# Kernel optimization log

Hardware: AMD Instinct MI355X
Metric: run time of the kernel (lower is better)

Reference implementation:

```python
import jax, jax.numpy as jnp
import numpy as np

T_BINS = 1000  # max_time_bins
N_HEADS = 8
BIN = 64


def _ln(x, g, b):
    m = x.mean(-1, keepdims=True)
    v = ((x - m) ** 2).mean(-1, keepdims=True)
    return (x - m) / jnp.sqrt(v + 1e-5) * g + b


def _time_attn(h, td, mask, wq, bq, wk, bk, wv, bv, wo, bo, temb):
    # h: [B,S,D], td: [B,S] float, mask: [B,S] bool
    B, S, D = h.shape
    dk = D // N_HEADS
    q = (h @ wq + bq).reshape(B, S, N_HEADS, dk)
    k = (h @ wk + bk).reshape(B, S, N_HEADS, dk)
    v = (h @ wv + bv).reshape(B, S, N_HEADS, dk)
    scores = jnp.einsum('bqhd,bkhd->bhqk', q, k) / jnp.sqrt(jnp.float32(dk))
    tb = jnp.clip(td.astype(jnp.int32), 0, T_BINS - 1)
    bias = temb[tb].transpose(0, 2, 1)[:, :, None, :]  # [B,H,1,S], key-position bias
    scores = jnp.where(mask[:, None, None, :], scores + bias, -1e9)
    attn = jax.nn.softmax(scores, axis=-1)
    ctx = jnp.einsum('bhqk,bkhd->bqhd', attn, v).reshape(B, S, D)
    return ctx @ wo + bo


def _forward(x, time_deltas,
             emb_event, emb_rel, emb_abs,
             iq_w, iq_b, ik_w, ik_b, iv_w, iv_b, io_w, io_b, i_temb, i_g, i_bt,
             eq_w, eq_b, ek_w, ek_b, ev_w, ev_b, eo_w, eo_b, e_temb, e_g, e_bt,
             w1, b1, w2, b2):
    B, S = x.shape
    NB = S // BIN  # S chosen as a multiple of bin_size -> no padding
    mask = x != 0  # padding_idx = 0
    ee = emb_event.at[0].set(0.0)  # padding_idx row is zero
    rel_bins = jnp.clip(time_deltas.astype(jnp.int32), 0, T_BINS - 1)
    abs_t = jnp.cumsum(jnp.clip(time_deltas, 0.0, None), axis=1)
    abs_bins = jnp.clip(abs_t.astype(jnp.int32), 0, T_BINS - 1)
    h = ee[x] + emb_rel[rel_bins] + emb_abs[abs_bins]  # [B,S,D]
    D = h.shape[-1]
    # intra-bin attention over [B*NB, BIN]
    hi = h.reshape(B * NB, BIN, D)
    ti = time_deltas.reshape(B * NB, BIN)
    mi = mask.reshape(B * NB, BIN)
    hi = _ln(_time_attn(hi, ti, mi, iq_w, iq_b, ik_w, ik_b, iv_w, iv_b, io_w, io_b, i_temb), i_g, i_bt)
    hi = hi.reshape(B, NB, BIN, D)
    # mean pool per bin over valid tokens
    mb = mask.reshape(B, NB, BIN)
    w = mb[..., None].astype(h.dtype)
    denom = jnp.maximum(w.sum(2), 1.0)
    bin_repr = (hi * w).sum(2) / denom  # [B,NB,D]
    bin_mask = mb.any(2)
    abs_masked = jnp.where(mb, abs_t.reshape(B, NB, BIN), 0.0)
    bin_abs = abs_masked.max(2)
    bin_rel = jnp.concatenate(
        [jnp.zeros((B, 1), h.dtype), jnp.maximum(bin_abs[:, 1:] - bin_abs[:, :-1], 0.0)], axis=1)
    h_inter = _ln(_time_attn(bin_repr, bin_rel, bin_mask,
                             eq_w, eq_b, ek_w, ek_b, ev_w, ev_b, eo_w, eo_b, e_temb), e_g, e_bt)
    last_idx = jnp.clip(bin_mask.sum(1) - 1, 0, None)
    last = h_inter[jnp.arange(B), last_idx]  # [B,D]
    return jax.nn.sigmoid(jax.nn.relu(last @ w1 + b1) @ w2 + b2)  # [B,1]


def setup_inputs() -> dict:
    key = jax.random.key(0)
    ks = jax.random.split(key, 24)
    B, S, D, V = 8, 4096, 512, 20000
    sc = 1.0 / np.sqrt(D)
    f32 = jnp.float32
    inp = {
        'x': jax.random.randint(ks[0], (B, S), 0, V),
        'time_deltas': jax.random.uniform(ks[1], (B, S), f32) * 10.0,
        'emb_event': jax.random.normal(ks[2], (V, D), f32) * 0.02,
        'emb_rel': jax.random.normal(ks[3], (T_BINS, D), f32) * 0.02,
        'emb_abs': jax.random.normal(ks[4], (T_BINS, D), f32) * 0.02,
    }
    names = ['iq', 'ik', 'iv', 'io', 'eq', 'ek', 'ev', 'eo']
    for i, n in enumerate(names):
        inp[n + '_w'] = jax.random.normal(ks[5 + i], (D, D), f32) * sc
        inp[n + '_b'] = jnp.zeros((D,), f32)
    inp['i_temb'] = jax.random.normal(ks[13], (T_BINS, N_HEADS), f32) * 0.02
    inp['e_temb'] = jax.random.normal(ks[14], (T_BINS, N_HEADS), f32) * 0.02
    inp['i_g'] = jnp.ones((D,), f32); inp['i_bt'] = jnp.zeros((D,), f32)
    inp['e_g'] = jnp.ones((D,), f32); inp['e_bt'] = jnp.zeros((D,), f32)
    inp['w1'] = jax.random.normal(ks[15], (D, D // 2), f32) * sc
    inp['b1'] = jnp.zeros((D // 2,), f32)
    inp['w2'] = jax.random.normal(ks[16], (D // 2, 1), f32) * np.sqrt(2.0 / D)
    inp['b2'] = jnp.zeros((1,), f32)
    return inp


def reference(x, time_deltas, emb_event, emb_rel, emb_abs,
              iq_w, iq_b, ik_w, ik_b, iv_w, iv_b, io_w, io_b, i_temb, i_g, i_bt,
              eq_w, eq_b, ek_w, ek_b, ev_w, ev_b, eo_w, eo_b, e_temb, e_g, e_bt,
              w1, b1, w2, b2):
    return _forward(x, time_deltas, emb_event, emb_rel, emb_abs,
                    iq_w, iq_b, ik_w, ik_b, iv_w, iv_b, io_w, io_b, i_temb, i_g, i_bt,
                    eq_w, eq_b, ek_w, ek_b, ev_w, ev_b, eo_w, eo_b, e_temb, e_g, e_bt,
                    w1, b1, w2, b2)
```

## Files before the change

kernel.cpp:

```cpp
#include <hip/hip_runtime.h>


typedef __attribute__((ext_vector_type(8))) short bf16x8;
typedef __attribute__((ext_vector_type(4))) float f32x4;
typedef __attribute__((ext_vector_type(4))) int i32x4;

#define DEVI __device__ __forceinline__

DEVI unsigned short f2bf(float f) {
  union { float f; unsigned u; } v; v.f = f;
  unsigned r = v.u + 0x7FFFu + ((v.u >> 16) & 1u);
  return (unsigned short)(r >> 16);
}
DEVI float bf2f(unsigned short u) {
  union { unsigned u; float f; } v; v.u = ((unsigned)u) << 16; return v.f;
}

#define GLOAD_LDS16(gp, lp) \
  __builtin_amdgcn_global_load_lds((const __attribute__((address_space(1))) void*)(gp), \
                                   (__attribute__((address_space(3))) void*)(lp), 16, 0, 0)

struct TPackArgs { const float* s[8]; unsigned short* d[8];
                   const float* bs[6]; float* bd[2]; };

__global__ __launch_bounds__(256) void k_tpack8(TPackArgs args) {
  __shared__ float tile[64][65];
  if (blockIdx.x == 512) {
    int t = threadIdx.x;
    for (int i = t; i < 1536; i += 256) {
      int sel = i >> 9, r = i & 511;
      args.bd[0][i] = args.bs[sel][r];
      args.bd[1][i] = args.bs[3 + sel][r];
    }
    return;
  }
  int mat = blockIdx.x >> 6;
  int tl = blockIdx.x & 63;
  const float* W = args.s[mat];
  unsigned short* Wt = args.d[mat];
  int n0 = (tl & 7) << 6, k0 = (tl >> 3) << 6;
  int t = threadIdx.x, j = t & 63, i0 = t >> 6;
#pragma unroll
  for (int rr = 0; rr < 16; ++rr) {
    int i = rr * 4 + i0;
    tile[i][j] = W[(size_t)(k0 + i) * 512 + n0 + j];
  }
  __syncthreads();
#pragma unroll
  for (int rr = 0; rr < 16; ++rr) {
    int i = rr * 4 + i0;
    Wt[(size_t)(n0 + i) * 512 + k0 + j] = f2bf(tile[j][i]);
  }
}

__global__ __launch_bounds__(64) void k_time(const float* __restrict__ td, const int* __restrict__ x,
    float* __restrict__ abs_t, float* __restrict__ bin_rel, int* __restrict__ bin_mask,
    int* __restrict__ last_idx) {
  __shared__ float tds[4096];
  __shared__ int xs[4096];
  int b = blockIdx.x, lane = threadIdx.x;
  const f32x4* tp = (const f32x4*)(td + (size_t)b * 4096);
  const i32x4* xp = (const i32x4*)(x + (size_t)b * 4096);
  for (int j = lane; j < 1024; j += 64) {
    f32x4 v = tp[j];
#pragma unroll
    for (int c = 0; c < 4; ++c) v[c] = fmaxf(v[c], 0.f);
    *(f32x4*)&tds[j * 4] = v;
    *(i32x4*)&xs[j * 4] = xp[j];
  }
  __syncthreads();
  float s = 0.f;
  for (int i = 0; i < 64; ++i) s += tds[lane * 64 + i];
  float pre = s;
#pragma unroll
  for (int off = 1; off < 64; off <<= 1) {
    float n = __shfl_up(pre, off, 64);
    if (lane >= off) pre += n;
  }
  float a = pre - s;
  float am = 0.f; int anyv = 0;
  for (int i = 0; i < 64; ++i) {
    a += tds[lane * 64 + i];
    tds[lane * 64 + i] = a;
    if (xs[lane * 64 + i] != 0) { am = fmaxf(am, a); anyv = 1; }
  }
  __syncthreads();
  float* out = abs_t + (size_t)b * 4096;
  for (int j = lane; j < 1024; j += 64)
    *(f32x4*)&out[j * 4] = *(const f32x4*)&tds[j * 4];
  float prev = __shfl_up(am, 1, 64);
  bin_rel[b * 64 + lane] = (lane == 0) ? 0.f : fmaxf(am - prev, 0.f);
  bin_mask[b * 64 + lane] = anyv;
  unsigned long long bal = __ballot(anyv != 0);
  if (lane == 0) last_idx[b] = max(__popcll(bal) - 1, 0);
}

__global__ __launch_bounds__(256) void k_embed(const int* __restrict__ x, const float* __restrict__ td,
    const float* __restrict__ abs_t, const float* __restrict__ ee, const float* __restrict__ er,
    const float* __restrict__ ea, unsigned short* __restrict__ h) {
  int t = threadIdx.x;
  int lane = t & 63;
  int c0 = lane * 8;
#pragma unroll
  for (int it = 0; it < 4; ++it) {
    int tok = blockIdx.x * 16 + it * 4 + (t >> 6);
    int xi = x[tok];
    int rb = (int)td[tok]; rb = min(max(rb, 0), 999);
    int ab = (int)abs_t[tok]; ab = min(max(ab, 0), 999);
    const f32x4* pr = (const f32x4*)(er + (size_t)rb * 512 + c0);
    const f32x4* pa = (const f32x4*)(ea + (size_t)ab * 512 + c0);
    f32x4 s0 = pr[0] + pa[0];
    f32x4 s1 = pr[1] + pa[1];
    if (xi != 0) {
      const f32x4* pe = (const f32x4*)(ee + (size_t)xi * 512 + c0);
      s0 += pe[0]; s1 += pe[1];
    }
    bf16x8 o;
#pragma unroll
    for (int i = 0; i < 4; ++i) { o[i] = (short)f2bf(s0[i]); o[4 + i] = (short)f2bf(s1[i]); }
    *(bf16x8*)(h + (size_t)tok * 512 + c0) = o;
  }
}

DEVI bf16x8 lds_frag32(const unsigned short* buf, int r, int g) {
  int sr = r >> 1;
  int slot = (((r & 1) << 2) | g) ^ (sr & 7);
  return *(const bf16x8*)&buf[sr * 64 + slot * 8];
}
DEVI bf16x8 lds_frag64(const unsigned short* buf, int row, int c) {
  return *(const bf16x8*)&buf[row * 64 + ((c ^ (row & 7)) << 3)];
}

__global__ __launch_bounds__(512, 2) void k_gemm256(const unsigned short* __restrict__ A,
    const unsigned short* __restrict__ Wt, const float* __restrict__ bias,
    unsigned short* __restrict__ Cout, int N, int tiles_n) {
  __shared__ unsigned short lds[4][2][256 * 32];
  int bid = blockIdx.x;
  { int q = (int)gridDim.x >> 3; bid = (bid & 7) * q + (bid >> 3); }
  int by = bid / tiles_n, bx = bid % tiles_n;
  int m0 = by << 8, n0 = bx << 8;
  int t = threadIdx.x;
  int lane = t & 63, w = t >> 6;
  int wm = w >> 2, wn = w & 3;
  int l15 = lane & 15, l4 = lane >> 4;

  auto stageA = [&](int kt) {
    int k0 = kt << 5;
    unsigned short* dst = &lds[kt & 3][0][0];
#pragma unroll
    for (int l = 0; l < 2; ++l) {
      int pos = l * 512 + t;
      int sr = pos >> 3, slot = pos & 7;
      int gp = slot ^ (sr & 7);
      int row = sr * 2 + (gp >> 2);
      GLOAD_LDS16(&A[(size_t)(m0 + row) * 512 + k0 + (gp & 3) * 8], dst + pos * 8);
    }
  };
  auto stageB = [&](int kt) {
    int k0 = kt << 5;
    unsigned short* dst = &lds[kt & 3][1][0];
#pragma unroll
    for (int l = 0; l < 2; ++l) {
      int pos = l * 512 + t;
      int sr = pos >> 3, slot = pos & 7;
      int gp = slot ^ (sr & 7);
      int row = sr * 2 + (gp >> 2);
      GLOAD_LDS16(&Wt[(size_t)(n0 + row) * 512 + k0 + (gp & 3) * 8], dst + pos * 8);
    }
  };

  f32x4 acc[8][4] = {};
  stageA(0); stageB(0);
  stageA(1); stageB(1);
  stageA(2); stageB(2);

  for (int kt = 0; kt < 16; ++kt) {
    if (kt < 14)       asm volatile("s_waitcnt vmcnt(8)" ::: "memory");
    else if (kt == 14) asm volatile("s_waitcnt vmcnt(4)" ::: "memory");
    else               asm volatile("s_waitcnt vmcnt(0)" ::: "memory");
    __builtin_amdgcn_s_barrier();
    const unsigned short* As = &lds[kt & 3][0][0];
    const unsigned short* Bs = &lds[kt & 3][1][0];

    bf16x8 af[4], bb[4];
#pragma unroll
    for (int i = 0; i < 4; ++i) af[i] = lds_frag32(As, wm * 128 + i * 16 + l15, l4);
#pragma unroll
    for (int j = 0; j < 4; ++j) bb[j] = lds_frag32(Bs, wn * 64 + j * 16 + l15, l4);
    if (kt < 13) stageA(kt + 3);
    __builtin_amdgcn_s_barrier();
    asm volatile("s_waitcnt lgkmcnt(0)" ::: "memory");
    __builtin_amdgcn_sched_barrier(0);
    __builtin_amdgcn_s_setprio(1);
#pragma unroll
    for (int i = 0; i < 4; ++i)
#pragma unroll
      for (int j = 0; j < 4; ++j)
        acc[i][j] = __builtin_amdgcn_mfma_f32_16x16x32_bf16(af[i], bb[j], acc[i][j], 0, 0, 0);
    __builtin_amdgcn_s_setprio(0);

    bf16x8 ah[4];
#pragma unroll
    for (int i = 0; i < 4; ++i) ah[i] = lds_frag32(As, wm * 128 + 64 + i * 16 + l15, l4);
    if (kt < 13) stageB(kt + 3);
    __builtin_amdgcn_s_barrier();
    asm volatile("s_waitcnt lgkmcnt(0)" ::: "memory");
    __builtin_amdgcn_sched_barrier(0);
    __builtin_amdgcn_s_setprio(1);
#pragma unroll
    for (int i = 0; i < 4; ++i)
#pragma unroll
      for (int j = 0; j < 4; ++j)
        acc[4 + i][j] = __builtin_amdgcn_mfma_f32_16x16x32_bf16(ah[i], bb[j], acc[4 + i][j], 0, 0, 0);
    __builtin_amdgcn_s_setprio(0);
  }

  __syncthreads();
  unsigned short* scr = ((unsigned short*)lds) + (size_t)w * 4352;
  float bov[4];
#pragma unroll
  for (int j = 0; j < 4; ++j) bov[j] = bias[n0 + wn * 64 + j * 16 + l15];
#pragma unroll
  for (int c = 0; c < 2; ++c) {
#pragma unroll
    for (int i = 0; i < 4; ++i)
#pragma unroll
      for (int j = 0; j < 4; ++j)
#pragma unroll
        for (int r = 0; r < 4; ++r)
          scr[(i * 16 + l4 * 4 + r) * 68 + j * 16 + l15] = f2bf(acc[c * 4 + i][j][r] + bov[j]);
#pragma unroll
    for (int p = 0; p < 8; ++p) {
      int rl = p * 8 + (lane >> 3);
      bf16x8 vv = *(const bf16x8*)&scr[rl * 68 + (lane & 7) * 8];
      *(bf16x8*)&Cout[(size_t)(m0 + wm * 128 + c * 64 + rl) * N + n0 + wn * 64 + (lane & 7) * 8] = vv;
    }
  }
}

__global__ __launch_bounds__(512, 2) void k_oproj(const unsigned short* __restrict__ ctx,
    const unsigned short* __restrict__ WoT, const float* __restrict__ bo,
    const int* __restrict__ x, const float* __restrict__ g, const float* __restrict__ bt,
    unsigned short* __restrict__ bin_repr) {
  __shared__ unsigned short As[128 * 64];
  __shared__ unsigned short Bs[512 * 64];
  int bid = blockIdx.x;
  { int q = (int)gridDim.x >> 3; bid = (bid & 7) * q + (bid >> 3); }
  int m0 = bid << 7;
  int t = threadIdx.x;
  int lane = t & 63, w = t >> 6;
  int l15 = lane & 15, l4 = lane >> 4;

  f32x4 acc[8][4] = {};
  for (int k0 = 0; k0 < 512; k0 += 64) {
    __syncthreads();
#pragma unroll
    for (int l = 0; l < 2; ++l) {
      int pos = l * 512 + t;
      int row = pos >> 3, gg = (pos & 7) ^ (row & 7);
      GLOAD_LDS16(&ctx[(size_t)(m0 + row) * 512 + k0 + gg * 8], &As[pos * 8]);
    }
#pragma unroll
    for (int l = 0; l < 8; ++l) {
      int pos = l * 512 + t;
      int row = pos >> 3, gg = (pos & 7) ^ (row & 7);
      GLOAD_LDS16(&WoT[(size_t)row * 512 + k0 + gg * 8], &Bs[pos * 8]);
    }
    __syncthreads();
#pragma unroll
    for (int ks = 0; ks < 2; ++ks) {
      bf16x8 af[8], bb[4];
#pragma unroll
      for (int i = 0; i < 8; ++i) af[i] = lds_frag64(As, i * 16 + l15, ks * 4 + l4);
#pragma unroll
      for (int j = 0; j < 4; ++j) bb[j] = lds_frag64(Bs, w * 64 + j * 16 + l15, ks * 4 + l4);
#pragma unroll
      for (int i = 0; i < 8; ++i)
#pragma unroll
        for (int j = 0; j < 4; ++j)
          acc[i][j] = __builtin_amdgcn_mfma_f32_16x16x32_bf16(af[i], bb[j], acc[i][j], 0, 0, 0);
    }
  }

  __syncthreads();
  float* red   = (float*)&As[0];
  float* meanL = red + 128 * 9;
  float* rstdL = meanL + 128;
  int*   valL  = (int*)(rstdL + 128);
  int*   cntL  = valL + 128;

  int cols[4]; float bov[4], gv[4], bv[4];
#pragma unroll
  for (int j = 0; j < 4; ++j) {
    cols[j] = w * 64 + j * 16 + l15;
    bov[j] = bo[cols[j]]; gv[j] = g[cols[j]]; bv[j] = bt[cols[j]];
  }
  if (t < 128) {
    int v = (x[m0 + t] != 0) ? 1 : 0;
    valL[t] = v;
    unsigned long long bal = __ballot(v != 0);
    if ((t & 63) == 0) cntL[t >> 6] = __popcll(bal);
  }
#pragma unroll
  for (int i = 0; i < 8; ++i)
#pragma unroll
    for (int r = 0; r < 4; ++r) {
      float s = (acc[i][0][r] + bov[0]) + (acc[i][1][r] + bov[1]) +
                (acc[i][2][r] + bov[2]) + (acc[i][3][r] + bov[3]);
#pragma unroll
      for (int off = 1; off < 16; off <<= 1) s += __shfl_xor(s, off, 64);
      if (l15 == 0) red[(i * 16 + l4 * 4 + r) * 9 + w] = s;
    }
  __syncthreads();
  if (t < 128) {
    float m = 0.f;
#pragma unroll
    for (int ww = 0; ww < 8; ++ww) m += red[t * 9 + ww];
    meanL[t] = m * (1.f / 512.f);
  }
  __syncthreads();
#pragma unroll
  for (int i = 0; i < 8; ++i)
#pragma unroll
    for (int r = 0; r < 4; ++r) {
      float m = meanL[i * 16 + l4 * 4 + r];
      float s = 0.f;
#pragma unroll
      for (int j = 0; j < 4; ++j) { float d = acc[i][j][r] + bov[j] - m; s += d * d; }
#pragma unroll
      for (int off = 1; off < 16; off <<= 1) s += __shfl_xor(s, off, 64);
      if (l15 == 0) red[(i * 16 + l4 * 4 + r) * 9 + w] = s;
    }
  __syncthreads();
  if (t < 128) {
    float vsum = 0.f;
#pragma unroll
    for (int ww = 0; ww < 8; ++ww) vsum += red[t * 9 + ww];
    rstdL[t] = rsqrtf(vsum * (1.f / 512.f) + 1e-5f);
  }
  __syncthreads();
  float p0[4] = {0.f, 0.f, 0.f, 0.f}, p1[4] = {0.f, 0.f, 0.f, 0.f};
#pragma unroll
  for (int i = 0; i < 8; ++i)
#pragma unroll
    for (int r = 0; r < 4; ++r) {
      int row = i * 16 + l4 * 4 + r;
      if (valL[row]) {
        float m = meanL[row], rs = rstdL[row];
#pragma unroll
        for (int j = 0; j < 4; ++j) {
          float y = (acc[i][j][r] + bov[j] - m) * rs * gv[j] + bv[j];
          if (i < 4) p0[j] += y; else p1[j] += y;
        }
      }
    }
#pragma unroll
  for (int j = 0; j < 4; ++j) {
    p0[j] += __shfl_xor(p0[j], 16, 64); p0[j] += __shfl_xor(p0[j], 32, 64);
    p1[j] += __shfl_xor(p1[j], 16, 64); p1[j] += __shfl_xor(p1[j], 32, 64);
  }
  float d0 = 1.f / fmaxf((float)cntL[0], 1.f);
  float d1 = 1.f / fmaxf((float)cntL[1], 1.f);
  if (l4 == 0) {
    int binr = (m0 >> 6);
#pragma unroll
    for (int j = 0; j < 4; ++j) {
      bin_repr[(size_t)binr * 512 + cols[j]]       = f2bf(p0[j] * d0);
      bin_repr[(size_t)(binr + 1) * 512 + cols[j]] = f2bf(p1[j] * d1);
    }
  }
}

__global__ __launch_bounds__(256) void k_gemm(const unsigned short* __restrict__ A,
    const unsigned short* __restrict__ Wt, const float* __restrict__ bias,
    unsigned short* __restrict__ Cout, int N, int tiles_n) {
  __shared__ unsigned short As[128 * 72];
  __shared__ unsigned short Bs[128 * 72];
  int bx = blockIdx.x % tiles_n;
  int by = blockIdx.x / tiles_n;
  int m0 = by << 7, n0 = bx << 7;
  int t = threadIdx.x;
  int lane = t & 63, w = t >> 6;
  int wm = w >> 1, wn = w & 1;
  f32x4 acc[4][4] = {};
  for (int k0 = 0; k0 < 512; k0 += 64) {
    __syncthreads();
#pragma unroll
    for (int i = 0; i < 4; ++i) {
      int idx = t + i * 256;
      int row = idx >> 3, seg = idx & 7;
      *(bf16x8*)&As[row * 72 + seg * 8] = *(const bf16x8*)&A[(size_t)(m0 + row) * 512 + k0 + seg * 8];
      *(bf16x8*)&Bs[row * 72 + seg * 8] = *(const bf16x8*)&Wt[(size_t)(n0 + row) * 512 + k0 + seg * 8];
    }
    __syncthreads();
#pragma unroll
    for (int ks = 0; ks < 2; ++ks) {
      bf16x8 af[4], bb[4];
#pragma unroll
      for (int i = 0; i < 4; ++i) {
        af[i] = *(const bf16x8*)&As[(wm * 64 + i * 16 + (lane & 15)) * 72 + ks * 32 + (lane >> 4) * 8];
        bb[i] = *(const bf16x8*)&Bs[(wn * 64 + i * 16 + (lane & 15)) * 72 + ks * 32 + (lane >> 4) * 8];
      }
#pragma unroll
      for (int i = 0; i < 4; ++i)
#pragma unroll
        for (int j = 0; j < 4; ++j)
          acc[i][j] = __builtin_amdgcn_mfma_f32_16x16x32_bf16(af[i], bb[j], acc[i][j], 0, 0, 0);
    }
  }
#pragma unroll
  for (int i = 0; i < 4; ++i) {
    int rowb = m0 + wm * 64 + i * 16 + ((lane >> 4) << 2);
#pragma unroll
    for (int j = 0; j < 4; ++j) {
      int col = n0 + wn * 64 + j * 16 + (lane & 15);
      float bv = bias[col];
#pragma unroll
      for (int r = 0; r < 4; ++r)
        Cout[(size_t)(rowb + r) * N + col] = f2bf(acc[i][j][r] + bv);
    }
  }
}

__global__ __launch_bounds__(256) void k_attn(const unsigned short* __restrict__ qkv,
    const float* __restrict__ td, const int* __restrict__ validv,
    const float* __restrict__ temb, unsigned short* __restrict__ ctx) {
  __shared__ float bias_s[4][64];
  __shared__ int valid_s[64];
  __shared__ unsigned short P_s[4][64][72];
  __shared__ unsigned short Vt_s[4][64][72];
  int blk = blockIdx.x >> 1, hg = blockIdx.x & 1;
  int t = threadIdx.x, hl = t >> 6, lane = t & 63;
  int h = hg * 4 + hl;
  size_t base = (size_t)blk * 64;
  if (t < 64) {
    valid_s[t] = (validv[base + t] != 0) ? 1 : 0;
    int tb = (int)td[base + t];
    tb = min(max(tb, 0), 999);
#pragma unroll
    for (int hh = 0; hh < 4; ++hh) bias_s[hh][t] = temb[tb * 8 + hg * 4 + hh];
  }
  {
    const unsigned short* vp = qkv + (base + lane) * 1536 + 1024 + h * 64;
#pragma unroll
    for (int f8 = 0; f8 < 8; ++f8) {
      bf16x8 v8 = *(const bf16x8*)(vp + f8 * 8);
#pragma unroll
      for (int j = 0; j < 8; ++j) Vt_s[hl][f8 * 8 + j][lane] = (unsigned short)v8[j];
    }
  }
  __syncthreads();
  bf16x8 qa[2][4], kb[2][4];
#pragma unroll
  for (int ks = 0; ks < 2; ++ks)
#pragma unroll
    for (int i = 0; i < 4; ++i) {
      int row = i * 16 + (lane & 15);
      int kk = ks * 32 + (lane >> 4) * 8;
      qa[ks][i] = *(const bf16x8*)&qkv[(base + row) * 1536 + h * 64 + kk];
      kb[ks][i] = *(const bf16x8*)&qkv[(base + row) * 1536 + 512 + h * 64 + kk];
    }
  f32x4 acc[4][4] = {};
#pragma unroll
  for (int ks = 0; ks < 2; ++ks)
#pragma unroll
    for (int i = 0; i < 4; ++i)
#pragma unroll
      for (int j = 0; j < 4; ++j)
        acc[i][j] = __builtin_amdgcn_mfma_f32_16x16x32_bf16(qa[ks][i], kb[ks][j], acc[i][j], 0, 0, 0);
  float invs[4][4];
#pragma unroll
  for (int i = 0; i < 4; ++i) {
#pragma unroll
    for (int r = 0; r < 4; ++r) {
      float sv[4];
#pragma unroll
      for (int j = 0; j < 4; ++j) {
        int key = j * 16 + (lane & 15);
        float s = acc[i][j][r] * 0.125f;
        sv[j] = valid_s[key] ? (s + bias_s[hl][key]) : -1e9f;
      }
      float m = fmaxf(fmaxf(sv[0], sv[1]), fmaxf(sv[2], sv[3]));
#pragma unroll
      for (int off = 1; off < 16; off <<= 1) m = fmaxf(m, __shfl_xor(m, off, 64));
      float p[4], sum = 0.f;
#pragma unroll
      for (int j = 0; j < 4; ++j) { p[j] = __expf(sv[j] - m); sum += p[j]; }
#pragma unroll
      for (int off = 1; off < 16; off <<= 1) sum += __shfl_xor(sum, off, 64);
      invs[i][r] = 1.f / sum;
      int row = i * 16 + ((lane >> 4) << 2) + r;
#pragma unroll
      for (int j = 0; j < 4; ++j) P_s[hl][row][j * 16 + (lane & 15)] = f2bf(p[j]);
    }
  }
  __syncthreads();
  f32x4 acc2[4][4] = {};
#pragma unroll
  for (int ks = 0; ks < 2; ++ks) {
    bf16x8 pa[4], vb[4];
    int kk = ks * 32 + (lane >> 4) * 8;
#pragma unroll
    for (int i = 0; i < 4; ++i) {
      pa[i] = *(const bf16x8*)&P_s[hl][i * 16 + (lane & 15)][kk];
      vb[i] = *(const bf16x8*)&Vt_s[hl][i * 16 + (lane & 15)][kk];
    }
#pragma unroll
    for (int i = 0; i < 4; ++i)
#pragma unroll
      for (int j = 0; j < 4; ++j)
        acc2[i][j] = __builtin_amdgcn_mfma_f32_16x16x32_bf16(pa[i], vb[j], acc2[i][j], 0, 0, 0);
  }
  unsigned short* scr = &Vt_s[hl][0][0];
#pragma unroll
  for (int i = 0; i < 4; ++i)
#pragma unroll
    for (int j = 0; j < 4; ++j)
#pragma unroll
      for (int r = 0; r < 4; ++r)
        scr[(i * 16 + ((lane >> 4) << 2) + r) * 72 + j * 16 + (lane & 15)] =
            f2bf(acc2[i][j][r] * invs[i][r]);
#pragma unroll
  for (int p = 0; p < 8; ++p) {
    int rl = p * 8 + (lane >> 3);
    bf16x8 vv = *(const bf16x8*)&scr[rl * 72 + (lane & 7) * 8];
    *(bf16x8*)&ctx[(base + rl) * 512 + h * 64 + (lane & 7) * 8] = vv;
  }
}

__global__ __launch_bounds__(256) void k_final(const unsigned short* __restrict__ proj2,
    const int* __restrict__ last_idx, const float* __restrict__ g, const float* __restrict__ bt,
    const float* __restrict__ w1, const float* __restrict__ b1,
    const float* __restrict__ w2, const float* __restrict__ b2, float* __restrict__ outp) {
  __shared__ float row_s[512];
  __shared__ float red_s[4];
  __shared__ float red2_s[4];
  int b = blockIdx.x, t = threadIdx.x;
  const unsigned short* rp = proj2 + (size_t)(b * 64 + last_idx[b]) * 512;
  float v0 = bf2f(rp[t]), v1 = bf2f(rp[t + 256]);
  float s = v0 + v1;
#pragma unroll
  for (int off = 1; off < 64; off <<= 1) s += __shfl_xor(s, off, 64);
  if ((t & 63) == 0) red_s[t >> 6] = s;
  __syncthreads();
  float mean = (red_s[0] + red_s[1] + red_s[2] + red_s[3]) * (1.f / 512.f);
  float d0 = v0 - mean, d1 = v1 - mean;
  float vs = d0 * d0 + d1 * d1;
#pragma unroll
  for (int off = 1; off < 64; off <<= 1) vs += __shfl_xor(vs, off, 64);
  if ((t & 63) == 0) red2_s[t >> 6] = vs;
  __syncthreads();
  float rstd = rsqrtf((red2_s[0] + red2_s[1] + red2_s[2] + red2_s[3]) * (1.f / 512.f) + 1e-5f);
  row_s[t]       = d0 * rstd * g[t]       + bt[t];
  row_s[t + 256] = d1 * rstd * g[t + 256] + bt[t + 256];
  __syncthreads();
  float acc = b1[t];
  for (int k = 0; k < 512; ++k) acc += row_s[k] * w1[(size_t)k * 256 + t];
  float hv = fmaxf(acc, 0.f) * w2[t];
#pragma unroll
  for (int off = 1; off < 64; off <<= 1) hv += __shfl_xor(hv, off, 64);
  if ((t & 63) == 0) red_s[t >> 6] = hv;
  __syncthreads();
  if (t == 0) {
    float o = red_s[0] + red_s[1] + red_s[2] + red_s[3] + b2[0];
    outp[b] = 1.f / (1.f + __expf(-o));
  }
}

extern "C" void kernel_launch(void* const* d_in, const int* in_sizes, int n_in,
                              void* d_out, int out_size, void* d_ws, size_t ws_size,
                              hipStream_t stream) {
  const int*   x    = (const int*)d_in[0];
  const float* td   = (const float*)d_in[1];
  const float* ee   = (const float*)d_in[2];
  const float* er   = (const float*)d_in[3];
  const float* ea   = (const float*)d_in[4];
  const float* iq_w = (const float*)d_in[5];  const float* iq_b = (const float*)d_in[6];
  const float* ik_w = (const float*)d_in[7];  const float* ik_b = (const float*)d_in[8];
  const float* iv_w = (const float*)d_in[9];  const float* iv_b = (const float*)d_in[10];
  const float* io_w = (const float*)d_in[11]; const float* io_b = (const float*)d_in[12];
  const float* eq_w = (const float*)d_in[13]; const float* eq_b = (const float*)d_in[14];
  const float* ek_w = (const float*)d_in[15]; const float* ek_b = (const float*)d_in[16];
  const float* ev_w = (const float*)d_in[17]; const float* ev_b = (const float*)d_in[18];
  const float* eo_w = (const float*)d_in[19]; const float* eo_b = (const float*)d_in[20];
  const float* i_temb = (const float*)d_in[21];
  const float* e_temb = (const float*)d_in[22];
  const float* i_g  = (const float*)d_in[23]; const float* i_bt = (const float*)d_in[24];
  const float* e_g  = (const float*)d_in[25]; const float* e_bt = (const float*)d_in[26];
  const float* w1   = (const float*)d_in[27]; const float* b1   = (const float*)d_in[28];
  const float* w2   = (const float*)d_in[29]; const float* b2   = (const float*)d_in[30];

  char* ws = (char*)d_ws;
  size_t off = 0;
  auto alloc = [&](size_t nb) { size_t r = off; off += (nb + 255) & ~(size_t)255; return r; };
  float* abs_t    = (float*)(ws + alloc((size_t)32768 * 4));
  float* bin_rel  = (float*)(ws + alloc(512 * 4));
  int*   bin_mask = (int*)(ws + alloc(512 * 4));
  int*   last_idx = (int*)(ws + alloc(64));
  unsigned short* wqkv_i = (unsigned short*)(ws + alloc((size_t)1536 * 512 * 2));
  unsigned short* wo_i   = (unsigned short*)(ws + alloc((size_t)512 * 512 * 2));
  unsigned short* wqkv_e = (unsigned short*)(ws + alloc((size_t)1536 * 512 * 2));
  unsigned short* wo_e   = (unsigned short*)(ws + alloc((size_t)512 * 512 * 2));
  float* bqkv_i = (float*)(ws + alloc(1536 * 4));
  float* bqkv_e = (float*)(ws + alloc(1536 * 4));
  unsigned short* hbuf = (unsigned short*)(ws + alloc((size_t)32768 * 512 * 2));
  unsigned short* qkvbuf = (unsigned short*)(ws + alloc((size_t)32768 * 1536 * 2));
  unsigned short* bin_repr = (unsigned short*)(ws + alloc((size_t)512 * 512 * 2));
  char* small = ws + alloc((size_t)512 * 1536 * 2);
  unsigned short* qkv2 = (unsigned short*)small;
  unsigned short* proj2 = (unsigned short*)small;
  unsigned short* ctx2 = (unsigned short*)(ws + alloc((size_t)512 * 512 * 2));

  TPackArgs tp;
  tp.s[0] = iq_w; tp.d[0] = wqkv_i;
  tp.s[1] = ik_w; tp.d[1] = wqkv_i + (size_t)512 * 512;
  tp.s[2] = iv_w; tp.d[2] = wqkv_i + (size_t)1024 * 512;
  tp.s[3] = io_w; tp.d[3] = wo_i;
  tp.s[4] = eq_w; tp.d[4] = wqkv_e;
  tp.s[5] = ek_w; tp.d[5] = wqkv_e + (size_t)512 * 512;
  tp.s[6] = ev_w; tp.d[6] = wqkv_e + (size_t)1024 * 512;
  tp.s[7] = eo_w; tp.d[7] = wo_e;
  tp.bs[0] = iq_b; tp.bs[1] = ik_b; tp.bs[2] = iv_b;
  tp.bs[3] = eq_b; tp.bs[4] = ek_b; tp.bs[5] = ev_b;
  tp.bd[0] = bqkv_i; tp.bd[1] = bqkv_e;
  k_tpack8<<<513, 256, 0, stream>>>(tp);

  k_time<<<8, 64, 0, stream>>>(td, x, abs_t, bin_rel, bin_mask, last_idx);

  k_embed<<<2048, 256, 0, stream>>>(x, td, abs_t, ee, er, ea, hbuf);

  k_gemm256<<<128 * 6, 512, 0, stream>>>(hbuf, wqkv_i, bqkv_i, qkvbuf, 1536, 6);
  k_attn<<<1024, 256, 0, stream>>>(qkvbuf, td, x, i_temb, hbuf);
  k_oproj<<<256, 512, 0, stream>>>(hbuf, wo_i, io_b, x, i_g, i_bt, bin_repr);

  k_gemm<<<4 * 12, 256, 0, stream>>>(bin_repr, wqkv_e, bqkv_e, qkv2, 1536, 12);
  k_attn<<<16, 256, 0, stream>>>(qkv2, bin_rel, bin_mask, e_temb, ctx2);
  k_gemm<<<4 * 4, 256, 0, stream>>>(ctx2, wo_e, eo_b, proj2, 512, 4);

  k_final<<<8, 256, 0, stream>>>(proj2, last_idx, e_g, e_bt, w1, b1, w2, b2, (float*)d_out);
}
```

Baseline: 237.7 us.

## Fuse intra-bin attention with output projection, LayerNorm and mean pooling

Merges the intra-bin attention kernel and the o-proj/LayerNorm/pool kernel into one kernel per 64-token bin. Each of the 8 waves handles one head, keeps its context in LDS, then multiplies it by Wo read directly from global memory. This removes the ctx round-trip through global memory and one launch. The gemm and attention epilogues also drop LDS-staged coalesced stores in favour of direct scattered 2-byte stores. Costs: Wo is re-read per block without LDS staging, the stores are less coalesced, and the large LDS footprint lowers occupancy.

```diff
diff --git a/kernel.cpp b/kernel.cpp
--- a/kernel.cpp
+++ b/kernel.cpp
@@ -127,9 +127,6 @@
   int slot = (((r & 1) << 2) | g) ^ (sr & 7);
   return *(const bf16x8*)&buf[sr * 64 + slot * 8];
 }
-DEVI bf16x8 lds_frag64(const unsigned short* buf, int row, int c) {
-  return *(const bf16x8*)&buf[row * 64 + ((c ^ (row & 7)) << 3)];
-}
 
 __global__ __launch_bounds__(512, 2) void k_gemm256(const unsigned short* __restrict__ A,
     const unsigned short* __restrict__ Wt, const float* __restrict__ bias,
@@ -214,160 +211,224 @@
         acc[4 + i][j] = __builtin_amdgcn_mfma_f32_16x16x32_bf16(ah[i], bb[j], acc[4 + i][j], 0, 0, 0);
     __builtin_amdgcn_s_setprio(0);
   }
-
-  __syncthreads();
-  unsigned short* scr = ((unsigned short*)lds) + (size_t)w * 4352;
-  float bov[4];
-#pragma unroll
-  for (int j = 0; j < 4; ++j) bov[j] = bias[n0 + wn * 64 + j * 16 + l15];
-#pragma unroll
-  for (int c = 0; c < 2; ++c) {
+#pragma unroll
+  for (int i = 0; i < 8; ++i) {
+    int rowb = m0 + wm * 128 + i * 16 + (l4 << 2);
+#pragma unroll
+    for (int j = 0; j < 4; ++j) {
+      int col = n0 + wn * 64 + j * 16 + l15;
+      float bv = bias[col];
+#pragma unroll
+      for (int r = 0; r < 4; ++r)
+        Cout[(size_t)(rowb + r) * N + col] = f2bf(acc[i][j][r] + bv);
+    }
+  }
+}
+
+__global__ __launch_bounds__(512) void k_attnproj(const unsigned short* __restrict__ qkv,
+    const float* __restrict__ td, const int* __restrict__ x, const float* __restrict__ temb,
+    const unsigned short* __restrict__ WoT, const float* __restrict__ bo,
+    const float* __restrict__ g, const float* __restrict__ bt,
+    unsigned short* __restrict__ bin_repr) {
+  __shared__ unsigned short Vt[8][64][72];
+  __shared__ unsigned short PsCtx[8 * 64 * 72];
+  __shared__ float bias_s[8][64];
+  __shared__ int valid_s[64];
+  __shared__ float red[64][9];
+  __shared__ float meanL[64];
+  __shared__ float rstdL[64];
+  __shared__ int cntS;
+  int blk = blockIdx.x;
+  int t = threadIdx.x, w = t >> 6, lane = t & 63;
+  int l15 = lane & 15, l4 = lane >> 4;
+  size_t base = (size_t)blk * 64;
+
+  if (t < 64) {
+    int v = (x[base + t] != 0) ? 1 : 0;
+    valid_s[t] = v;
+    int tb = (int)td[base + t];
+    tb = min(max(tb, 0), 999);
+#pragma unroll
+    for (int hh = 0; hh < 8; ++hh) bias_s[hh][t] = temb[tb * 8 + hh];
+    unsigned long long bal = __ballot(v != 0);
+    if (t == 0) cntS = __popcll(bal);
+  }
+  {
+    const unsigned short* vp = qkv + (base + lane) * 1536 + 1024 + w * 64;
+#pragma unroll
+    for (int f8 = 0; f8 < 8; ++f8) {
+      bf16x8 v8 = *(const bf16x8*)(vp + f8 * 8);
+#pragma unroll
+      for (int j = 0; j < 8; ++j) Vt[w][f8 * 8 + j][lane] = (unsigned short)v8[j];
+    }
+  }
+  __syncthreads();
+
+  bf16x8 qa[2][4], kb[2][4];
+#pragma unroll
+  for (int ks = 0; ks < 2; ++ks)
+#pragma unroll
+    for (int i = 0; i < 4; ++i) {
+      int row = i * 16 + l15;
+      int kk = ks * 32 + l4 * 8;
+      qa[ks][i] = *(const bf16x8*)&qkv[(base + row) * 1536 + w * 64 + kk];
+      kb[ks][i] = *(const bf16x8*)&qkv[(base + row) * 1536 + 512 + w * 64 + kk];
+    }
+  f32x4 acc[4][4] = {};
+#pragma unroll
+  for (int ks = 0; ks < 2; ++ks)
 #pragma unroll
     for (int i = 0; i < 4; ++i)
 #pragma unroll
       for (int j = 0; j < 4; ++j)
-#pragma unroll
-        for (int r = 0; r < 4; ++r)
-          scr[(i * 16 + l4 * 4 + r) * 68 + j * 16 + l15] = f2bf(acc[c * 4 + i][j][r] + bov[j]);
-#pragma unroll
-    for (int p = 0; p < 8; ++p) {
-      int rl = p * 8 + (lane >> 3);
-      bf16x8 vv = *(const bf16x8*)&scr[rl * 68 + (lane & 7) * 8];
-      *(bf16x8*)&Cout[(size_t)(m0 + wm * 128 + c * 64 + rl) * N + n0 + wn * 64 + (lane & 7) * 8] = vv;
-    }
-  }
-}
-
-__global__ __launch_bounds__(512, 2) void k_oproj(const unsigned short* __restrict__ ctx,
-    const unsigned short* __restrict__ WoT, const float* __restrict__ bo,
-    const int* __restrict__ x, const float* __restrict__ g, const float* __restrict__ bt,
-    unsigned short* __restrict__ bin_repr) {
-  __shared__ unsigned short As[128 * 64];
-  __shared__ unsigned short Bs[512 * 64];
-  int bid = blockIdx.x;
-  { int q = (int)gridDim.x >> 3; bid = (bid & 7) * q + (bid >> 3); }
-  int m0 = bid << 7;
-  int t = threadIdx.x;
-  int lane = t & 63, w = t >> 6;
-  int l15 = lane & 15, l4 = lane >> 4;
-
-  f32x4 acc[8][4] = {};
-  for (int k0 = 0; k0 < 512; k0 += 64) {
-    __syncthreads();
-#pragma unroll
-    for (int l = 0; l < 2; ++l) {
-      int pos = l * 512 + t;
-      int row = pos >> 3, gg = (pos & 7) ^ (row & 7);
-      GLOAD_LDS16(&ctx[(size_t)(m0 + row) * 512 + k0 + gg * 8], &As[pos * 8]);
-    }
-#pragma unroll
-    for (int l = 0; l < 8; ++l) {
-      int pos = l * 512 + t;
-      int row = pos >> 3, gg = (pos & 7) ^ (row & 7);
-      GLOAD_LDS16(&WoT[(size_t)row * 512 + k0 + gg * 8], &Bs[pos * 8]);
-    }
-    __syncthreads();
+        acc[i][j] = __builtin_amdgcn_mfma_f32_16x16x32_bf16(qa[ks][i], kb[ks][j], acc[i][j], 0, 0, 0);
+
+  unsigned short* Psw = &PsCtx[w * 64 * 72];
+  float invs[4][4];
+#pragma unroll
+  for (int i = 0; i < 4; ++i) {
+#pragma unroll
+    for (int r = 0; r < 4; ++r) {
+      float sv[4];
+#pragma unroll
+      for (int j = 0; j < 4; ++j) {
+        int key = j * 16 + l15;
+        float s = acc[i][j][r] * 0.125f;
+        sv[j] = valid_s[key] ? (s + bias_s[w][key]) : -1e9f;
+      }
+      float m = fmaxf(fmaxf(sv[0], sv[1]), fmaxf(sv[2], sv[3]));
+#pragma unroll
+      for (int off = 1; off < 16; off <<= 1) m = fmaxf(m, __shfl_xor(m, off, 64));
+      float p[4], sum = 0.f;
+#pragma unroll
+      for (int j = 0; j < 4; ++j) { p[j] = __expf(sv[j] - m); sum += p[j]; }
+#pragma unroll
+      for (int off = 1; off < 16; off <<= 1) sum += __shfl_xor(sum, off, 64);
+      invs[i][r] = 1.f / sum;
+      int row = i * 16 + l4 * 4 + r;
+#pragma unroll
+      for (int j = 0; j < 4; ++j) Psw[row * 72 + j * 16 + l15] = f2bf(p[j]);
+    }
+  }
+
+  f32x4 acc2[4][4] = {};
+#pragma unroll
+  for (int ks = 0; ks < 2; ++ks) {
+    bf16x8 pa[4], vb[4];
+    int kk = ks * 32 + l4 * 8;
+#pragma unroll
+    for (int i = 0; i < 4; ++i) {
+      pa[i] = *(const bf16x8*)&Psw[(i * 16 + l15) * 72 + kk];
+      vb[i] = *(const bf16x8*)&Vt[w][i * 16 + l15][kk];
+    }
+#pragma unroll
+    for (int i = 0; i < 4; ++i)
+#pragma unroll
+      for (int j = 0; j < 4; ++j)
+        acc2[i][j] = __builtin_amdgcn_mfma_f32_16x16x32_bf16(pa[i], vb[j], acc2[i][j], 0, 0, 0);
+  }
+
+  __syncthreads();
+  unsigned short* ctxl = PsCtx;
+#pragma unroll
+  for (int i = 0; i < 4; ++i)
+#pragma unroll
+    for (int j = 0; j < 4; ++j)
+#pragma unroll
+      for (int r = 0; r < 4; ++r)
+        ctxl[(i * 16 + l4 * 4 + r) * 520 + w * 64 + j * 16 + l15] =
+            f2bf(acc2[i][j][r] * invs[i][r]);
+  __syncthreads();
+
+  int n0 = w * 64;
+  f32x4 acc3[4][4] = {};
+#pragma unroll
+  for (int kb = 0; kb < 8; ++kb)
 #pragma unroll
     for (int ks = 0; ks < 2; ++ks) {
-      bf16x8 af[8], bb[4];
-#pragma unroll
-      for (int i = 0; i < 8; ++i) af[i] = lds_frag64(As, i * 16 + l15, ks * 4 + l4);
-#pragma unroll
-      for (int j = 0; j < 4; ++j) bb[j] = lds_frag64(Bs, w * 64 + j * 16 + l15, ks * 4 + l4);
-#pragma unroll
-      for (int i = 0; i < 8; ++i)
+      int kk = kb * 64 + ks * 32 + l4 * 8;
+      bf16x8 af[4], bb[4];
+#pragma unroll
+      for (int i = 0; i < 4; ++i) af[i] = *(const bf16x8*)&ctxl[(i * 16 + l15) * 520 + kk];
+#pragma unroll
+      for (int j = 0; j < 4; ++j)
+        bb[j] = *(const bf16x8*)&WoT[(size_t)(n0 + j * 16 + l15) * 512 + kk];
+#pragma unroll
+      for (int i = 0; i < 4; ++i)
 #pragma unroll
         for (int j = 0; j < 4; ++j)
-          acc[i][j] = __builtin_amdgcn_mfma_f32_16x16x32_bf16(af[i], bb[j], acc[i][j], 0, 0, 0);
-    }
-  }
-
-  __syncthreads();
-  float* red   = (float*)&As[0];
-  float* meanL = red + 128 * 9;
-  float* rstdL = meanL + 128;
-  int*   valL  = (int*)(rstdL + 128);
-  int*   cntL  = valL + 128;
-
-  int cols[4]; float bov[4], gv[4], bv[4];
+          acc3[i][j] = __builtin_amdgcn_mfma_f32_16x16x32_bf16(af[i], bb[j], acc3[i][j], 0, 0, 0);
+    }
+
+  float bov[4], gv[4], bv[4];
 #pragma unroll
   for (int j = 0; j < 4; ++j) {
-    cols[j] = w * 64 + j * 16 + l15;
-    bov[j] = bo[cols[j]]; gv[j] = g[cols[j]]; bv[j] = bt[cols[j]];
-  }
-  if (t < 128) {
-    int v = (x[m0 + t] != 0) ? 1 : 0;
-    valL[t] = v;
-    unsigned long long bal = __ballot(v != 0);
-    if ((t & 63) == 0) cntL[t >> 6] = __popcll(bal);
-  }
-#pragma unroll
-  for (int i = 0; i < 8; ++i)
+    int col = n0 + j * 16 + l15;
+    bov[j] = bo[col]; gv[j] = g[col]; bv[j] = bt[col];
+  }
+#pragma unroll
+  for (int i = 0; i < 4; ++i)
 #pragma unroll
     for (int r = 0; r < 4; ++r) {
-      float s = (acc[i][0][r] + bov[0]) + (acc[i][1][r] + bov[1]) +
-                (acc[i][2][r] + bov[2]) + (acc[i][3][r] + bov[3]);
+      float s = (acc3[i][0][r] + bov[0]) + (acc3[i][1][r] + bov[1]) +
+                (acc3[i][2][r] + bov[2]) + (acc3[i][3][r] + bov[3]);
 #pragma unroll
       for (int off = 1; off < 16; off <<= 1) s += __shfl_xor(s, off, 64);
-      if (l15 == 0) red[(i * 16 + l4 * 4 + r) * 9 + w] = s;
-    }
-  __syncthreads();
-  if (t < 128) {
+      if (l15 == 0) red[i * 16 + l4 * 4 + r][w] = s;
+    }
+  __syncthreads();
+  if (t < 64) {
     float m = 0.f;
 #pragma unroll
-    for (int ww = 0; ww < 8; ++ww) m += red[t * 9 + ww];
+    for (int ww = 0; ww < 8; ++ww) m += red[t][ww];
     meanL[t] = m * (1.f / 512.f);
   }
   __syncthreads();
 #pragma unroll
-  for (int i = 0; i < 8; ++i)
+  for (int i = 0; i < 4; ++i)
 #pragma unroll
     for (int r = 0; r < 4; ++r) {
       float m = meanL[i * 16 + l4 * 4 + r];
       float s = 0.f;
 #pragma unroll
-      for (int j = 0; j < 4; ++j) { float d = acc[i][j][r] + bov[j] - m; s += d * d; }
+      for (int j = 0; j < 4; ++j) { float d = acc3[i][j][r] + bov[j] - m; s += d * d; }
 #pragma unroll
       for (int off = 1; off < 16; off <<= 1) s += __shfl_xor(s, off, 64);
-      if (l15 == 0) red[(i * 16 + l4 * 4 + r) * 9 + w] = s;
-    }
-  __syncthreads();
-  if (t < 128) {
+      if (l15 == 0) red[i * 16 + l4 * 4 + r][w] = s;
+    }
+  __syncthreads();
+  if (t < 64) {
     float vsum = 0.f;
 #pragma unroll
-    for (int ww = 0; ww < 8; ++ww) vsum += red[t * 9 + ww];
+    for (int ww = 0; ww < 8; ++ww) vsum += red[t][ww];
     rstdL[t] = rsqrtf(vsum * (1.f / 512.f) + 1e-5f);
   }
   __syncthreads();
-  float p0[4] = {0.f, 0.f, 0.f, 0.f}, p1[4] = {0.f, 0.f, 0.f, 0.f};
-#pragma unroll
-  for (int i = 0; i < 8; ++i)
+
+  float s4[4] = {0.f, 0.f, 0.f, 0.f};
+#pragma unroll
+  for (int i = 0; i < 4; ++i)
 #pragma unroll
     for (int r = 0; r < 4; ++r) {
       int row = i * 16 + l4 * 4 + r;
-      if (valL[row]) {
+      if (valid_s[row]) {
         float m = meanL[row], rs = rstdL[row];
 #pragma unroll
-        for (int j = 0; j < 4; ++j) {
-          float y = (acc[i][j][r] + bov[j] - m) * rs * gv[j] + bv[j];
-          if (i < 4) p0[j] += y; else p1[j] += y;
-        }
+        for (int j = 0; j < 4; ++j) s4[j] += (acc3[i][j][r] + bov[j] - m) * rs;
       }
     }
 #pragma unroll
   for (int j = 0; j < 4; ++j) {
-    p0[j] += __shfl_xor(p0[j], 16, 64); p0[j] += __shfl_xor(p0[j], 32, 64);
-    p1[j] += __shfl_xor(p1[j], 16, 64); p1[j] += __shfl_xor(p1[j], 32, 64);
-  }
-  float d0 = 1.f / fmaxf((float)cntL[0], 1.f);
-  float d1 = 1.f / fmaxf((float)cntL[1], 1.f);
+    s4[j] += __shfl_xor(s4[j], 16, 64);
+    s4[j] += __shfl_xor(s4[j], 32, 64);
+  }
+  int cnt = cntS;
+  float denom = fmaxf((float)cnt, 1.f);
   if (l4 == 0) {
-    int binr = (m0 >> 6);
-#pragma unroll
-    for (int j = 0; j < 4; ++j) {
-      bin_repr[(size_t)binr * 512 + cols[j]]       = f2bf(p0[j] * d0);
-      bin_repr[(size_t)(binr + 1) * 512 + cols[j]] = f2bf(p1[j] * d1);
-    }
+#pragma unroll
+    for (int j = 0; j < 4; ++j)
+      bin_repr[(size_t)blk * 512 + n0 + j * 16 + l15] =
+          f2bf((gv[j] * s4[j] + (float)cnt * bv[j]) / denom);
   }
 }
 
@@ -511,20 +572,16 @@
       for (int j = 0; j < 4; ++j)
         acc2[i][j] = __builtin_amdgcn_mfma_f32_16x16x32_bf16(pa[i], vb[j], acc2[i][j], 0, 0, 0);
   }
-  unsigned short* scr = &Vt_s[hl][0][0];
-#pragma unroll
-  for (int i = 0; i < 4; ++i)
-#pragma unroll
-    for (int j = 0; j < 4; ++j)
+#pragma unroll
+  for (int i = 0; i < 4; ++i) {
+    int rowb = i * 16 + ((lane >> 4) << 2);
+#pragma unroll
+    for (int j = 0; j < 4; ++j) {
+      int col = h * 64 + j * 16 + (lane & 15);
 #pragma unroll
       for (int r = 0; r < 4; ++r)
-        scr[(i * 16 + ((lane >> 4) << 2) + r) * 72 + j * 16 + (lane & 15)] =
-            f2bf(acc2[i][j][r] * invs[i][r]);
-#pragma unroll
-  for (int p = 0; p < 8; ++p) {
-    int rl = p * 8 + (lane >> 3);
-    bf16x8 vv = *(const bf16x8*)&scr[rl * 72 + (lane & 7) * 8];
-    *(bf16x8*)&ctx[(base + rl) * 512 + h * 64 + (lane & 7) * 8] = vv;
+        ctx[(base + rowb + r) * 512 + col] = f2bf(acc2[i][j][r] * invs[i][r]);
+    }
   }
 }
 
@@ -630,8 +687,7 @@
   k_embed<<<2048, 256, 0, stream>>>(x, td, abs_t, ee, er, ea, hbuf);
 
   k_gemm256<<<128 * 6, 512, 0, stream>>>(hbuf, wqkv_i, bqkv_i, qkvbuf, 1536, 6);
-  k_attn<<<1024, 256, 0, stream>>>(qkvbuf, td, x, i_temb, hbuf);
-  k_oproj<<<256, 512, 0, stream>>>(hbuf, wo_i, io_b, x, i_g, i_bt, bin_repr);
+  k_attnproj<<<512, 512, 0, stream>>>(qkvbuf, td, x, i_temb, wo_i, io_b, i_g, i_bt, bin_repr);
 
   k_gemm<<<4 * 12, 256, 0, stream>>>(bin_repr, wqkv_e, bqkv_e, qkv2, 1536, 12);
   k_attn<<<16, 256, 0, stream>>>(qkv2, bin_rel, bin_mask, e_temb, ctx2);
```

After: 239.3 us. Within noise of the previous version (+0.7%).
